# Performance work log

Hardware: AMD Instinct MI355X
Metric: run time of the kernel (lower is better)

## Reference

```python
import jax, jax.numpy as jnp
import numpy as np

VW, VD, VH = 96, 96, 96  # voxel_width, voxel_depth, voxel_height


def _grid_points():
    # voxel centers mapped to [-1, 1]: (2*i + 1 - N) / N
    xp = (2.0 * jnp.arange(VW) + 1.0 - VW) / VW
    yp = (2.0 * jnp.arange(VD) + 1.0 - VD) / VD
    zp = (2.0 * jnp.arange(VH) + 1.0 - VH) / VH
    X, Y, Z = jnp.meshgrid(xp, yp, zp, indexing='ij')
    return jnp.stack([X.ravel(), Y.ravel(), Z.ravel()], axis=-1)  # (V, 3)


def setup_inputs() -> dict:
    key = jax.random.key(0)
    k1, k2 = jax.random.split(key)
    B, NV, NF = 8, 2048, 512
    vertices = jax.random.uniform(k1, (B, NV, 3), dtype=jnp.float32, minval=-1.0, maxval=1.0)
    facets = jax.random.randint(k2, (B, NF, 4), 0, NV, dtype=jnp.int64)
    return {"vertices": vertices, "facets": facets}


def reference(vertices, facets):
    # vertices: (B, NV, 3) float32; facets: (B, NF, 4) int indices into vertices
    B = vertices.shape[0]
    NF = facets.shape[1]
    # vertices_to_facets: per-batch gather -> (B, NF, 4, 3)
    fverts = jax.vmap(lambda v, f: v[f])(vertices, facets)
    P = _grid_points()                      # (V, 3) voxel centers
    V = P.shape[0]

    def step(idx_map, xs):
        fi, verts = xs                      # verts: (B, 4, 3)
        v3 = verts[:, 3]                    # (B, 3)
        # T[:, j] = verts[j] - verts[3]  (columns are tetra edges)
        T = jnp.swapaxes(verts[:, :3] - v3[:, None, :], 1, 2)  # (B, 3, 3)
        a, b, c = T[:, 0, 0], T[:, 0, 1], T[:, 0, 2]
        d, e, f = T[:, 1, 0], T[:, 1, 1], T[:, 1, 2]
        g, h, i = T[:, 2, 0], T[:, 2, 1], T[:, 2, 2]
        # adjugate of T (matches t_inv_* in the original)
        adj = jnp.stack([
            jnp.stack([e * i - f * h, c * h - b * i, b * f - c * e], axis=-1),
            jnp.stack([f * g - d * i, a * i - c * g, c * d - a * f], axis=-1),
            jnp.stack([d * h - e * g, b * g - a * h, a * e - b * d], axis=-1),
        ], axis=1)                          # (B, 3, 3)
        det = a * (e * i - f * h) - b * (d * i - f * g) + c * (d * h - e * g)  # (B,)
        dvec = P[None, :, :] - v3[:, None, :]                  # (B, V, 3)
        lam = jnp.einsum('brc,bvc->bvr', adj, dvec) / det[:, None, None]  # (B, V, 3)
        lam4 = 1.0 - lam.sum(axis=-1, keepdims=True)
        lams = jnp.concatenate([lam, lam4], axis=-1)           # (B, V, 4)
        # original skips when any lambda < 0 or > 1 (strict) -> inside is inclusive
        inside = jnp.all((lams >= 0.0) & (lams <= 1.0), axis=-1)  # (B, V)
        idx_map = jnp.where((idx_map < 0) & inside, fi, idx_map)
        return idx_map, None

    idx0 = jnp.full((B, V), -1, dtype=jnp.int32)
    xs = (jnp.arange(NF, dtype=jnp.int32), jnp.swapaxes(fverts, 0, 1))
    idx_map, _ = jax.lax.scan(step, idx0, xs)
    alpha = (idx_map >= 0).astype(jnp.float32).reshape(B, VW, VD, VH)
    return alpha
```

## Files before the change

### kernel.cpp

```cpp
#include <hip/hip_runtime.h>

#pragma clang fp contract(off)

#define VWD 96
#define NVERT 2048
#define NFAC 512
#define NBATCH 8
#define NSLAB 3456
#define RECF 20
#define CULC 22

#define CUL(c, b, f) cul[(size_t)(c) * (NBATCH * NFAC) + (size_t)(b) * NFAC + (f)]

__global__ __launch_bounds__(512) void precompute_kernel(
    const float* __restrict__ vertices,
    const int*   __restrict__ facets,
    float*       __restrict__ cul,
    float*       __restrict__ body)
{
    __shared__ unsigned skey[NFAC];
    const int b = blockIdx.x;
    const int j = threadIdx.x;
    const float* vb = vertices + (size_t)b * NVERT * 3;

    int4 fi = ((const int4*)facets)[b * NFAC + j];
    float x0 = vb[3*fi.x+0], y0 = vb[3*fi.x+1], z0 = vb[3*fi.x+2];
    float x1 = vb[3*fi.y+0], y1 = vb[3*fi.y+1], z1 = vb[3*fi.y+2];
    float x2 = vb[3*fi.z+0], y2 = vb[3*fi.z+1], z2 = vb[3*fi.z+2];
    float x3 = vb[3*fi.w+0], y3 = vb[3*fi.w+1], z3 = vb[3*fi.w+2];
    float a  = x0-x3, bb = x1-x3, c  = x2-x3;
    float d  = y0-y3, e  = y1-y3, f  = y2-y3;
    float g  = z0-z3, h  = z1-z3, ii = z2-z3;
    float A00 = e*ii - f*h,  A01 = c*h  - bb*ii, A02 = bb*f - c*e;
    float A10 = f*g  - d*ii, A11 = a*ii - c*g,   A12 = c*d  - a*f;
    float A20 = d*h  - e*g,  A21 = bb*g - a*h,   A22 = a*e  - bb*d;
    float det = a*(e*ii - f*h) - bb*(d*ii - f*g) + c*(d*h - e*g);
    if (det < 0.0f) {
        det = -det;
        A00 = -A00; A01 = -A01; A02 = -A02;
        A10 = -A10; A11 = -A11; A12 = -A12;
        A20 = -A20; A21 = -A21; A22 = -A22;
    }
    unsigned myk = ~__float_as_uint(det);
    skey[j] = myk;
    __syncthreads();

    int rank = 0;
    const uint4* sk4 = (const uint4*)skey;
    for (int k0 = 0; k0 < NFAC; k0 += 4) {
        uint4 kk = sk4[k0 >> 2];
        rank += (kk.x < myk) + ((kk.x == myk) & (k0 + 0 < j));
        rank += (kk.y < myk) + ((kk.y == myk) & (k0 + 1 < j));
        rank += (kk.z < myk) + ((kk.z == myk) & (k0 + 2 < j));
        rank += (kk.w < myk) + ((kk.w == myk) & (k0 + 3 < j));
    }

    CUL(0, b, rank) = fminf(fminf(x0,x1),fminf(x2,x3)) - 1e-4f;
    CUL(1, b, rank) = fminf(fminf(y0,y1),fminf(y2,y3)) - 1e-4f;
    CUL(2, b, rank) = fminf(fminf(z0,z1),fminf(z2,z3)) - 1e-4f;
    CUL(3, b, rank) = fmaxf(fmaxf(x0,x1),fmaxf(x2,x3)) + 1e-4f;
    CUL(4, b, rank) = fmaxf(fmaxf(y0,y1),fmaxf(y2,y3)) + 1e-4f;
    CUL(5, b, rank) = fmaxf(fmaxf(z0,z1),fmaxf(z2,z3)) + 1e-4f;

    const float HX = 7.0f/96.0f, HZ = 3.0f/96.0f;
    auto plane = [&](float pax, float pay, float paz,
                     float pbx, float pby, float pbz,
                     float pcx, float pcy, float pcz,
                     float pox, float poy, float poz, int base) {
        float e1x = pbx-pax, e1y = pby-pay, e1z = pbz-paz;
        float e2x = pcx-pax, e2y = pcy-pay, e2z = pcz-paz;
        float nx = e1y*e2z - e1z*e2y;
        float ny = e1z*e2x - e1x*e2z;
        float nz = e1x*e2y - e1y*e2x;
        float sdot = nx*(pox-pax) + ny*(poy-pay) + nz*(poz-paz);
        if (sdot > 0.0f) { nx=-nx; ny=-ny; nz=-nz; sdot=-sdot; }
        float dpl = nx*pax + ny*pay + nz*paz;
        float n1s = fabsf(nx)+fabsf(ny)+fabsf(nz);
        float M = 1e-4f*(-sdot) + 1e-4f*n1s + 1e-4f;
        float rhs = dpl + M + (fabsf(nx)*HX + fabsf(ny)*HX + fabsf(nz)*HZ);
        CUL(base+0, b, rank) = nx;
        CUL(base+1, b, rank) = ny;
        CUL(base+2, b, rank) = nz;
        CUL(base+3, b, rank) = rhs;
    };
    plane(x1,y1,z1, x2,y2,z2, x3,y3,z3, x0,y0,z0, 6);
    plane(x0,y0,z0, x2,y2,z2, x3,y3,z3, x1,y1,z1, 10);
    plane(x0,y0,z0, x1,y1,z1, x3,y3,z3, x2,y2,z2, 14);
    plane(x0,y0,z0, x1,y1,z1, x2,y2,z2, x3,y3,z3, 18);

    const float DZ = 2.0f / 96.0f;
    float margA = det * 1e-4f + 1e-3f;
    float* bo = body + ((size_t)b * NFAC + rank) * RECF;
    bo[0]  = det; bo[1]  = x3;  bo[2]  = y3;  bo[3]  = z3;
    bo[4]  = A00; bo[5]  = A01; bo[6]  = A02;
    bo[7]  = A10; bo[8]  = A11; bo[9]  = A12;
    bo[10] = A20; bo[11] = A21; bo[12] = A22;
    bo[13] = margA;
    bo[14] = det - margA;
    bo[15] = det + margA;
    float ss0 = A02 * DZ, ss1 = A12 * DZ, ss2 = A22 * DZ;
    bo[16] = ss0; bo[17] = ss1; bo[18] = ss2;
    bo[19] = ss0 + ss1 + ss2;
}

__global__ __launch_bounds__(512) void mask_kernel(
    const float* __restrict__ cul,
    unsigned long long* __restrict__ masks)
{
    const int col = blockIdx.x;
    const int b   = blockIdx.y;
    const int f   = threadIdx.x;
    const int w   = threadIdx.x >> 6;
    float bminx=CUL(0,b,f), bminy=CUL(1,b,f), bminz=CUL(2,b,f);
    float bmaxx=CUL(3,b,f), bmaxy=CUL(4,b,f), bmaxz=CUL(5,b,f);
    float n0x=CUL(6,b,f),  n0y=CUL(7,b,f),  n0z=CUL(8,b,f),  r0=CUL(9,b,f);
    float n1x=CUL(10,b,f), n1y=CUL(11,b,f), n1z=CUL(12,b,f), r1=CUL(13,b,f);
    float n2x=CUL(14,b,f), n2y=CUL(15,b,f), n2z=CUL(16,b,f), r2=CUL(17,b,f);
    float n3x=CUL(18,b,f), n3y=CUL(19,b,f), n3z=CUL(20,b,f), r3=CUL(21,b,f);

    const int sx = col / 12, sy = col % 12;
    const float cx = (float)(16*sx + 8 - VWD) / 96.0f;
    const float cy = (float)(16*sy + 8 - VWD) / 96.0f;
    const float colminx = (float)(16*sx + 1  - VWD) / 96.0f;
    const float colmaxx = (float)(16*sx + 15 - VWD) / 96.0f;
    const float colminy = (float)(16*sy + 1  - VWD) / 96.0f;
    const float colmaxy = (float)(16*sy + 15 - VWD) / 96.0f;
    const bool ovxy = (bminx <= colmaxx) & (bmaxx >= colminx) &
                      (bminy <= colmaxy) & (bmaxy >= colminy);

    const float cz0   = (float)(4 - VWD) / 96.0f;
    const float stepc = 8.0f / 96.0f;
    float d0 = n0x*cx + n0y*cy + n0z*cz0 - r0;  float s0 = n0z*stepc;
    float d1 = n1x*cx + n1y*cy + n1z*cz0 - r1;  float s1 = n1z*stepc;
    float d2 = n2x*cx + n2y*cy + n2z*cz0 - r2;  float s2 = n2z*stepc;
    float d3 = n3x*cx + n3y*cy + n3z*cz0 - r3;  float s3 = n3z*stepc;
    float zlo = (float)(1 - VWD) / 96.0f;
    float zhi = (float)(7 - VWD) / 96.0f;

    unsigned long long* mp = masks + ((size_t)b * NSLAB + (size_t)col * 24) * 8 + w;
#pragma unroll 4
    for (int sz = 0; sz < 24; ++sz) {
        bool ov = ovxy & (bminz <= zhi) & (bmaxz >= zlo) &
                  (d0 <= 0.0f) & (d1 <= 0.0f) & (d2 <= 0.0f) & (d3 <= 0.0f);
        unsigned long long bal = __ballot((int)ov);
        if ((threadIdx.x & 63) == 0) mp[(size_t)sz * 8] = bal;
        d0 += s0; d1 += s1; d2 += s2; d3 += s3;
        zlo += stepc; zhi += stepc;
    }
}

__global__ __launch_bounds__(256) void voxelize_kernel(
    const float*              __restrict__ body,
    const unsigned long long* __restrict__ masks,
    float*                    __restrict__ out)
{
    const int b    = blockIdx.y;
    const int wave = threadIdx.x >> 6;
    const int lane = threadIdx.x & 63;
    const int slab = blockIdx.x * 4 + wave;
    const int sz = slab % 24;
    const int sy = (slab / 24) % 12;
    const int sx = slab / 288;
    const int ix  = sx*8 + (lane >> 3);
    const int iy  = sy*8 + (lane & 7);
    const int iz0 = sz*4;

    const float px  = (float)(2*ix  + 1 - VWD) / 96.0f;
    const float py  = (float)(2*iy  + 1 - VWD) / 96.0f;
    const float pz0 = (float)(2*iz0 + 1 - VWD) / 96.0f;

    const unsigned long long* mp = masks + ((size_t)b * NSLAB + slab) * 8;
    const float* bb = body + (size_t)b * NFAC * RECF;

    unsigned fnd = 0u;
    for (int w = 0; w < 8; ++w) {
        unsigned long long m = mp[w];
        while (m) {
            int bit = __builtin_ctzll(m);
            m &= m - 1;
            int f = __builtin_amdgcn_readfirstlane(w * 64 + bit);
            const float* bo = bb + f * RECF;
            float det = bo[0], v3x = bo[1], v3y = bo[2], v3z = bo[3];
            float A00 = bo[4],  A01 = bo[5],  A02 = bo[6];
            float A10 = bo[7],  A11 = bo[8],  A12 = bo[9];
            float A20 = bo[10], A21 = bo[11], A22 = bo[12];
            float margA = bo[13], dhi = bo[14], mhi = bo[15];
            float ss0 = bo[16], ss1 = bo[17], ss2 = bo[18], sss = bo[19];
            float dx = px - v3x, dy = py - v3y, dz0 = pz0 - v3z;
            float n0 = A00*dx + A01*dy + A02*dz0;
            float n1 = A10*dx + A11*dy + A12*dz0;
            float n2 = A20*dx + A21*dy + A22*dz0;
            float sm = n0 + n1 + n2;
            float nmargA = -margA;
#pragma unroll
            for (int k = 0; k < 4; ++k) {
                float mn = fminf(fminf(n0, n1), n2);
                bool def = (mn >= margA) & (sm <= dhi);
                bool may = (mn >= nmargA) & (sm <= mhi);
                bool needex = may & !def & !((fnd >> k) & 1u);
                if (__any(needex)) {
                    int izk = iz0 + k;
                    float pzk = (float)(2*izk + 1 - VWD) / 96.0f;
                    float dzk = pzk - v3z;
                    float e0 = A00*dx + A01*dy + A02*dzk;
                    float e1 = A10*dx + A11*dy + A12*dzk;
                    float e2 = A20*dx + A21*dy + A22*dzk;
                    float l0 = e0 / det;
                    float l1 = e1 / det;
                    float l2 = e2 / det;
                    float l3 = 1.0f - (l0 + l1 + l2);
                    bool inside = (l0 >= 0.0f) & (l0 <= 1.0f) &
                                  (l1 >= 0.0f) & (l1 <= 1.0f) &
                                  (l2 >= 0.0f) & (l2 <= 1.0f) &
                                  (l3 >= 0.0f) & (l3 <= 1.0f);
                    if (needex & inside) fnd |= (1u << k);
                }
                if (def) fnd |= (1u << k);
                if (k < 3) { n0 += ss0; n1 += ss1; n2 += ss2; sm += sss; }
            }
            if (__all(fnd == 15u)) goto done;
        }
    }
done:
    float4 v;
    v.x = (fnd & 1u) ? 1.0f : 0.0f;
    v.y = (fnd & 2u) ? 1.0f : 0.0f;
    v.z = (fnd & 4u) ? 1.0f : 0.0f;
    v.w = (fnd & 8u) ? 1.0f : 0.0f;
    *(float4*)&out[(size_t)b*(VWD*VWD*VWD) + (size_t)ix*(VWD*VWD) + iy*VWD + iz0] = v;
}

extern "C" void kernel_launch(void* const* d_in, const int* in_sizes, int n_in,
                              void* d_out, int out_size, void* d_ws, size_t ws_size,
                              hipStream_t stream) {
    const float* vertices = (const float*)d_in[0];
    const int*   facets   = (const int*)d_in[1];
    float*       out      = (float*)d_out;

    float* cul  = (float*)d_ws;
    float* body = (float*)((char*)d_ws + (size_t)CULC * NBATCH * NFAC * 4);
    unsigned long long* msk =
        (unsigned long long*)((char*)d_ws +
                              (size_t)(CULC + RECF) * NBATCH * NFAC * 4);

    precompute_kernel<<<NBATCH, 512, 0, stream>>>(vertices, facets, cul, body);
    mask_kernel<<<dim3(144, NBATCH), 512, 0, stream>>>(cul, msk);
    dim3 grid(NSLAB / 4, NBATCH);
    voxelize_kernel<<<grid, 256, 0, stream>>>(body, msk, out);
}
```

Measured before the change: 149.7 us.

## Scramble slab-to-wave mapping, preload mask words, and pair facet processing

Slab indices are permuted by a multiplicative hash (1537 mod 3456) so neighbouring waves take spatially distant slabs. This is meant to balance uneven per-slab facet counts across blocks and CUs. All eight mask words are now loaded up front instead of one per loop iteration. Facets are taken two at a time, which gives the compiler room to issue the second facet's record loads early, at the cost of more registers and a coarser early-exit check.

Measured after the change: 152.6 us. No clear change (+1.9%).

```diff
diff --git a/kernel.cpp b/kernel.cpp
--- a/kernel.cpp
+++ b/kernel.cpp
@@ -157,7 +157,8 @@
     const int b    = blockIdx.y;
     const int wave = threadIdx.x >> 6;
     const int lane = threadIdx.x & 63;
-    const int slab = blockIdx.x * 4 + wave;
+    const int raw  = blockIdx.x * 4 + wave;
+    const int slab = (raw * 1537) % NSLAB;
     const int sz = slab % 24;
     const int sy = (slab / 24) % 12;
     const int sx = slab / 288;
@@ -173,61 +174,86 @@
     const float* bb = body + (size_t)b * NFAC * RECF;
 
     unsigned fnd = 0u;
-    for (int w = 0; w < 8; ++w) {
-        unsigned long long m = mp[w];
+
+    auto process = [&](const float* __restrict__ bo) {
+        float det = bo[0], v3x = bo[1], v3y = bo[2], v3z = bo[3];
+        float A00 = bo[4],  A01 = bo[5],  A02 = bo[6];
+        float A10 = bo[7],  A11 = bo[8],  A12 = bo[9];
+        float A20 = bo[10], A21 = bo[11], A22 = bo[12];
+        float margA = bo[13], dhi = bo[14], mhi = bo[15];
+        float ss0 = bo[16], ss1 = bo[17], ss2 = bo[18], sss = bo[19];
+        float dx = px - v3x, dy = py - v3y, dz0 = pz0 - v3z;
+        float n0 = A00*dx + A01*dy + A02*dz0;
+        float n1 = A10*dx + A11*dy + A12*dz0;
+        float n2 = A20*dx + A21*dy + A22*dz0;
+        float sm = n0 + n1 + n2;
+        float nmargA = -margA;
+#pragma unroll
+        for (int k = 0; k < 4; ++k) {
+            float mn = fminf(fminf(n0, n1), n2);
+            bool def = (mn >= margA) & (sm <= dhi);
+            bool may = (mn >= nmargA) & (sm <= mhi);
+            bool needex = may & !def & !((fnd >> k) & 1u);
+            if (__any(needex)) {
+                int izk = iz0 + k;
+                float pzk = (float)(2*izk + 1 - VWD) / 96.0f;
+                float dzk = pzk - v3z;
+                float e0 = A00*dx + A01*dy + A02*dzk;
+                float e1 = A10*dx + A11*dy + A12*dzk;
+                float e2 = A20*dx + A21*dy + A22*dzk;
+                float l0 = e0 / det;
+                float l1 = e1 / det;
+                float l2 = e2 / det;
+                float l3 = 1.0f - (l0 + l1 + l2);
+                bool inside = (l0 >= 0.0f) & (l0 <= 1.0f) &
+                              (l1 >= 0.0f) & (l1 <= 1.0f) &
+                              (l2 >= 0.0f) & (l2 <= 1.0f) &
+                              (l3 >= 0.0f) & (l3 <= 1.0f);
+                if (needex & inside) fnd |= (1u << k);
+            }
+            if (def) fnd |= (1u << k);
+            if (k < 3) { n0 += ss0; n1 += ss1; n2 += ss2; sm += sss; }
+        }
+    };
+
+    auto processWord = [&](unsigned long long m, int base) -> bool {
         while (m) {
-            int bit = __builtin_ctzll(m);
-            m &= m - 1;
-            int f = __builtin_amdgcn_readfirstlane(w * 64 + bit);
-            const float* bo = bb + f * RECF;
-            float det = bo[0], v3x = bo[1], v3y = bo[2], v3z = bo[3];
-            float A00 = bo[4],  A01 = bo[5],  A02 = bo[6];
-            float A10 = bo[7],  A11 = bo[8],  A12 = bo[9];
-            float A20 = bo[10], A21 = bo[11], A22 = bo[12];
-            float margA = bo[13], dhi = bo[14], mhi = bo[15];
-            float ss0 = bo[16], ss1 = bo[17], ss2 = bo[18], sss = bo[19];
-            float dx = px - v3x, dy = py - v3y, dz0 = pz0 - v3z;
-            float n0 = A00*dx + A01*dy + A02*dz0;
-            float n1 = A10*dx + A11*dy + A12*dz0;
-            float n2 = A20*dx + A21*dy + A22*dz0;
-            float sm = n0 + n1 + n2;
-            float nmargA = -margA;
-#pragma unroll
-            for (int k = 0; k < 4; ++k) {
-                float mn = fminf(fminf(n0, n1), n2);
-                bool def = (mn >= margA) & (sm <= dhi);
-                bool may = (mn >= nmargA) & (sm <= mhi);
-                bool needex = may & !def & !((fnd >> k) & 1u);
-                if (__any(needex)) {
-                    int izk = iz0 + k;
-                    float pzk = (float)(2*izk + 1 - VWD) / 96.0f;
-                    float dzk = pzk - v3z;
-                    float e0 = A00*dx + A01*dy + A02*dzk;
-                    float e1 = A10*dx + A11*dy + A12*dzk;
-                    float e2 = A20*dx + A21*dy + A22*dzk;
-                    float l0 = e0 / det;
-                    float l1 = e1 / det;
-                    float l2 = e2 / det;
-                    float l3 = 1.0f - (l0 + l1 + l2);
-                    bool inside = (l0 >= 0.0f) & (l0 <= 1.0f) &
-                                  (l1 >= 0.0f) & (l1 <= 1.0f) &
-                                  (l2 >= 0.0f) & (l2 <= 1.0f) &
-                                  (l3 >= 0.0f) & (l3 <= 1.0f);
-                    if (needex & inside) fnd |= (1u << k);
-                }
-                if (def) fnd |= (1u << k);
-                if (k < 3) { n0 += ss0; n1 += ss1; n2 += ss2; sm += sss; }
+            int b0 = __builtin_ctzll(m); m &= m - 1;
+            int f0 = __builtin_amdgcn_readfirstlane(base + b0);
+            const float* bo0 = bb + f0 * RECF;
+            if (m) {
+                int b1 = __builtin_ctzll(m); m &= m - 1;
+                int f1 = __builtin_amdgcn_readfirstlane(base + b1);
+                const float* bo1 = bb + f1 * RECF;
+                process(bo0);
+                process(bo1);
+            } else {
+                process(bo0);
             }
-            if (__all(fnd == 15u)) goto done;
+            if (__all(fnd == 15u)) return true;
         }
-    }
+        return false;
+    };
+
+    unsigned long long m0 = mp[0], m1 = mp[1], m2 = mp[2], m3 = mp[3];
+    unsigned long long m4 = mp[4], m5 = mp[5], m6 = mp[6], m7 = mp[7];
+    if (processWord(m0,   0)) goto done;
+    if (processWord(m1,  64)) goto done;
+    if (processWord(m2, 128)) goto done;
+    if (processWord(m3, 192)) goto done;
+    if (processWord(m4, 256)) goto done;
+    if (processWord(m5, 320)) goto done;
+    if (processWord(m6, 384)) goto done;
+    if (processWord(m7, 448)) goto done;
 done:
-    float4 v;
-    v.x = (fnd & 1u) ? 1.0f : 0.0f;
-    v.y = (fnd & 2u) ? 1.0f : 0.0f;
-    v.z = (fnd & 4u) ? 1.0f : 0.0f;
-    v.w = (fnd & 8u) ? 1.0f : 0.0f;
-    *(float4*)&out[(size_t)b*(VWD*VWD*VWD) + (size_t)ix*(VWD*VWD) + iy*VWD + iz0] = v;
+    {
+        float4 v;
+        v.x = (fnd & 1u) ? 1.0f : 0.0f;
+        v.y = (fnd & 2u) ? 1.0f : 0.0f;
+        v.z = (fnd & 4u) ? 1.0f : 0.0f;
+        v.w = (fnd & 8u) ? 1.0f : 0.0f;
+        *(float4*)&out[(size_t)b*(VWD*VWD*VWD) + (size_t)ix*(VWD*VWD) + iy*VWD + iz0] = v;
+    }
 }
 
 extern "C" void kernel_launch(void* const* d_in, const int* in_sizes, int n_in,
```
